# Performance work log

Hardware: AMD Instinct MI355X
Metric: run time of the kernel (lower is better)

The kernel has to match this reference:

```python
import jax, jax.numpy as jnp
import numpy as np

D = 128        # feature dim (hard-coded 128 split in source)
C = 16         # number of classes
N_S = 1600     # support set size (C * 100 shots)
Q = 32768      # number of query samples
HID = 128      # Class_Adap hidden width


def _class_centers(support_feat_inv, support_features, support_labels):
    # per-class mean of both support tensors (ComputeClassCenters)
    ones = jnp.ones((support_labels.shape[0],), support_feat_inv.dtype)
    counts = jax.ops.segment_sum(ones, support_labels, num_segments=C)
    counts = jnp.maximum(counts, 1.0)[:, None]                     # [C,1]
    mean_s = jax.ops.segment_sum(support_feat_inv, support_labels, num_segments=C) / counts   # [C,D]
    pre_s = jax.ops.segment_sum(support_features, support_labels, num_segments=C) / counts    # [C,D]
    return mean_s, pre_s


def setup_inputs() -> dict:
    key = jax.random.key(0)
    ks = jax.random.split(key, 6)
    return {
        "support_feat_inv": jax.random.normal(ks[0], (N_S, D), jnp.float32),
        "support_features": jax.random.normal(ks[1], (N_S, D), jnp.float32),
        "query_features": jax.random.normal(ks[2], (Q, D), jnp.float32),
        "W1": jax.random.normal(ks[3], (2 * D + 1, HID), jnp.float32) * 0.05,
        "b1": jnp.zeros((HID,), jnp.float32),
        "W2": jax.random.normal(ks[4], (HID, 1), jnp.float32) * 0.05,
        "b2": jnp.zeros((1,), jnp.float32),
        "support_labels": jax.random.randint(ks[5], (N_S,), 0, C),
        "query_labels": jax.random.randint(jax.random.fold_in(key, 7), (Q,), 0, C),
    }


def reference(support_feat_inv, support_features, query_features, W1, b1, W2, b2,
              support_labels, query_labels) -> jnp.ndarray:
    mean_s, pre_s = _class_centers(support_feat_inv, support_features, support_labels)
    q = query_features[:, None, :]                                  # [Q,1,D]
    gated = jax.nn.sigmoid(mean_s)[None, :, :] * q                  # [Q,C,D]
    q_full = jnp.broadcast_to(q, gated.shape)                       # [Q,C,D]
    inp = jnp.concatenate([q_full, gated], axis=-1)                 # [Q,C,2D]
    # AdaptiveAvgPool2d((None, D)) on [C,1,2D]: average adjacent pairs along last dim
    pooled = inp.reshape(Q, C, D, 2).mean(axis=-1)                  # [Q,C,D]
    # inner/outer product: sum(pre_support * query) per class
    outer = jnp.sum(pre_s[None, :, :] * q, axis=-1, keepdims=True)  # [Q,C,1]
    ext = jnp.concatenate([inp, outer], axis=-1)                    # [Q,C,2D+1]
    # Class_Adap tiny MLP -> per-class scalar weight
    h = jax.nn.relu(jnp.einsum('qce,eh->qch', ext, W1) + b1)        # [Q,C,HID]
    w = jax.nn.sigmoid(jnp.einsum('qch,ho->qco', h, W2) + b2)       # [Q,C,1]
    agg = jnp.sum(pooled * w, axis=1)                               # [Q,D]
    return agg + query_features                                     # residual (query_feature[0])
```

## Files before the change

kernel.cpp:

```cpp
#include <hip/hip_runtime.h>
#include <hip/hip_bf16.h>
#include <stdint.h>

#define DD 128
#define CC 16
#define NS 1600
#define QQ 32768
#define NBLK 64
#define PLW 65

typedef __attribute__((ext_vector_type(8))) short short8;
typedef __attribute__((ext_vector_type(4))) short short4v;
typedef __attribute__((ext_vector_type(4))) float f32x4;

__device__ inline short f2bf(float x) {
  union { float f; uint32_t u; } v; v.f = x;
  uint32_t r = (v.u + 0x7FFFu + ((v.u >> 16) & 1u)) >> 16;
  return (short)r;
}

__device__ inline uint32_t pk2bf(float lo, float hi) {
  __hip_bfloat162 h = __float22bfloat162_rn(make_float2(lo, hi));
  union { __hip_bfloat162 h2; uint32_t u; } v; v.h2 = h;
  return v.u;
}

__device__ inline float bfbits2f(uint32_t hi16bits) {
  union { uint32_t u; float f; } v; v.u = hi16bits;
  return v.f;
}

__global__ __launch_bounds__(256) void prep_kernel(
    const float* __restrict__ sfi, const float* __restrict__ sf,
    const int* __restrict__ labels, const float* __restrict__ qf,
    float* __restrict__ partA, float* __restrict__ partB,
    float* __restrict__ pcnt, short* __restrict__ qbf) {
  const int t = threadIdx.x;

  if (blockIdx.x >= NBLK) {
    const size_t cb = (size_t)(blockIdx.x - NBLK) * (128 * DD);
#pragma unroll
    for (int i = 0; i < 16; ++i) {
      const size_t off = cb + ((size_t)i * 256 + t) * 4;
      f32x4 f = *(const f32x4*)(qf + off);
      union { short4v s; uint32_t u[2]; } r;
      r.u[0] = pk2bf(f[0], f[1]);
      r.u[1] = pk2bf(f[2], f[3]);
      *(short4v*)(qbf + off) = r.s;
    }
    return;
  }

  __shared__ float accA[2][CC][DD];
  __shared__ float accB[2][CC][DD];
  __shared__ float cnt[2][CC];
  const int d = t & 127, s = t >> 7;
  for (int i = t; i < 2 * CC * DD; i += 256) {
    ((float*)accA)[i] = 0.f;
    ((float*)accB)[i] = 0.f;
  }
  if (t < 2 * CC) ((float*)cnt)[t] = 0.f;
  __syncthreads();

  const int base = blockIdx.x * (NS / NBLK);
  for (int i = s; i < NS / NBLK; i += 2) {
    const int r = base + i;
    const int lbl = labels[r];
    accA[s][lbl][d] += sfi[(size_t)r * DD + d];
    accB[s][lbl][d] += sf[(size_t)r * DD + d];
    if (d == 0) cnt[s][lbl] += 1.f;
  }
  __syncthreads();

  float* pa = partA + (size_t)blockIdx.x * (CC * DD);
  float* pb = partB + (size_t)blockIdx.x * (CC * DD);
  for (int i = t; i < CC * DD; i += 256) {
    pa[i] = ((float*)accA)[i] + ((float*)accA)[CC * DD + i];
    pb[i] = ((float*)accB)[i] + ((float*)accB)[CC * DD + i];
  }
  if (t < CC) pcnt[blockIdx.x * CC + t] = cnt[0][t] + cnt[1][t];
}

__global__ __launch_bounds__(256) void build_wt_kernel(
    const float* __restrict__ W1, const float* __restrict__ partA,
    const float* __restrict__ partB, const float* __restrict__ pcnt,
    float* __restrict__ sg_out, short* __restrict__ WtTg) {
  __shared__ float sgc[DD], prc[DD];
  const int c = blockIdx.x, t = threadIdx.x;

  float cnt = 0.f;
  for (int b = 0; b < NBLK; ++b) cnt += pcnt[b * CC + c];
  cnt = fmaxf(cnt, 1.f);
  if (t < 128) {
    float a = 0.f;
    for (int b = 0; b < NBLK; ++b) a += partA[(size_t)b * (CC * DD) + c * DD + t];
    const float m = a / cnt;
    const float s = 1.f / (1.f + expf(-m));
    sgc[t] = s;
    sg_out[c * DD + t] = s;
  } else {
    const int d = t - 128;
    float a = 0.f;
    for (int b = 0; b < NBLK; ++b) a += partB[(size_t)b * (CC * DD) + c * DD + d];
    prc[d] = a / cnt;
  }
  __syncthreads();

  for (int it = 0; it < 8; ++it) {
    const int u = it * 256 + t;
    const int w_ = u >> 8;
    const int kb = (u >> 6) & 3;
    const int lane = u & 63;
    const int j = w_ * 16 + (lane & 15);
    const int e0 = kb * 32 + (lane >> 4) * 8;
    short8 r;
#pragma unroll
    for (int rr = 0; rr < 8; ++rr) {
      const int e = e0 + rr;
      float v = W1[e * DD + j] + sgc[e] * W1[(DD + e) * DD + j] +
                prc[e] * W1[2 * DD * DD + j];
      r[rr] = f2bf(v);
    }
    *(short8*)(WtTg + ((size_t)c * 2048 + u) * 8) = r;
  }
}

__global__ __launch_bounds__(512, 4) void main_kernel(
    const short* __restrict__ qbf, const short* __restrict__ WtTg,
    const float* __restrict__ b1, const float* __restrict__ W2,
    const float* __restrict__ b2, const float* __restrict__ sg,
    float* __restrict__ out) {
  __shared__ float p_pln[4 * 64 * PLW];
  __shared__ float w_lds[64][17];

  const int tid = threadIdx.x;
  const int lane = tid & 63;
  const int w = tid >> 6;
  const int l15 = lane & 15, l4 = lane >> 4;
  const int qbase = blockIdx.x * 64;

  short8 bq[4][4];
#pragma unroll
  for (int qn = 0; qn < 4; ++qn) {
    const short* qrow = qbf + (size_t)(qbase + qn * 16 + l15) * DD;
#pragma unroll
    for (int kb = 0; kb < 4; ++kb)
      bq[qn][kb] = *(const short8*)(qrow + kb * 32 + l4 * 8);
  }

  const f32x4 b1v = *(const f32x4*)(b1 + w * 16 + l4 * 4);
  const f32x4 w2v = *(const f32x4*)(W2 + w * 16 + l4 * 4);
  const float b2s = b2[0];

  const char* wbase = (const char*)WtTg + w * 4096 + lane * 16;

#define LOADW(dst, cls)                                                     \
  {                                                                         \
    _Pragma("unroll") for (int kb = 0; kb < 4; ++kb) dst[kb] =              \
        *(const short8*)(wbase + (size_t)(cls)*32768 + kb * 1024);          \
  }

#define COMPUTE(wf, cls)                                                    \
  {                                                                         \
    const int slot = (((cls)&7) * 8 + w) * PLW + lane;                      \
    _Pragma("unroll") for (int qp = 0; qp < 2; ++qp) {                      \
      f32x4 a0 = b1v, a1 = b1v;                                             \
      _Pragma("unroll") for (int kb = 0; kb < 4; ++kb) {                    \
        a0 = __builtin_amdgcn_mfma_f32_16x16x32_bf16(wf[kb],                \
                                                     bq[2 * qp][kb], a0,    \
                                                     0, 0, 0);              \
        a1 = __builtin_amdgcn_mfma_f32_16x16x32_bf16(wf[kb],                \
                                                     bq[2 * qp + 1][kb],    \
                                                     a1, 0, 0, 0);          \
      }                                                                     \
      float p0 = 0.f, p1 = 0.f;                                             \
      _Pragma("unroll") for (int i = 0; i < 4; ++i) {                       \
        p0 += fmaxf(a0[i], 0.f) * w2v[i];                                   \
        p1 += fmaxf(a1[i], 0.f) * w2v[i];                                   \
      }                                                                     \
      p_pln[(2 * qp) * (64 * PLW) + slot] = p0;                             \
      p_pln[(2 * qp + 1) * (64 * PLW) + slot] = p1;                         \
    }                                                                       \
  }

#define REDUCE(hf)                                                          \
  {                                                                         \
    __syncthreads();                                                        \
    if (tid < 256) {                                                        \
      const int qp = tid >> 7, c7 = (tid >> 4) & 7, lr = tid & 15;          \
      _Pragma("unroll") for (int qq = 0; qq < 2; ++qq) {                    \
        const int qn = qp * 2 + qq;                                         \
        const float* pb = p_pln + qn * (64 * PLW) + c7 * (8 * PLW) + lr;    \
        float sacc = 0.f;                                                   \
        _Pragma("unroll") for (int wv = 0; wv < 8; ++wv)                    \
            _Pragma("unroll") for (int g = 0; g < 4; ++g) sacc +=           \
            pb[wv * PLW + g * 16];                                          \
        w_lds[qn * 16 + lr][(hf)*8 + c7] =                                  \
            1.f / (1.f + __expf(-(sacc + b2s)));                            \
      }                                                                     \
    }                                                                       \
    __syncthreads();                                                        \
  }

  short8 wfA[4], wfB[4];
  LOADW(wfA, 0);
  for (int cp = 0; cp < CC; cp += 2) {
    LOADW(wfB, cp + 1);
    COMPUTE(wfA, cp);
    if (cp + 2 < CC) LOADW(wfA, cp + 2);
    COMPUTE(wfB, cp + 1);
    if (cp == 6) REDUCE(0);
    if (cp == 14) REDUCE(1);
  }
#undef LOADW
#undef COMPUTE
#undef REDUCE

  {
    float2 sgv[16];
#pragma unroll
    for (int c = 0; c < 16; ++c)
      sgv[c] = *(const float2*)(sg + c * DD + 2 * lane);

#pragma unroll
    for (int qi = 0; qi < 8; ++qi) {
      const int ql = qi * 8 + w;
      const int q = qbase + ql;
      float Sv = 0.f, swx = 0.f, swy = 0.f;
#pragma unroll
      for (int c = 0; c < 16; ++c) {
        const float wc = w_lds[ql][c];
        Sv += wc;
        swx += wc * sgv[c].x;
        swy += wc * sgv[c].y;
      }
      const uint16_t* row = (const uint16_t*)(qbf + (size_t)q * DD);
      const uint32_t pair = *(const uint32_t*)(row + 2 * lane);
      const float q0 = bfbits2f(pair << 16);
      const float q1 = bfbits2f(pair & 0xFFFF0000u);
      const float qlo = bfbits2f((uint32_t)row[lane] << 16);
      const float qhi = bfbits2f((uint32_t)row[64 + lane] << 16);

      float* orow = out + (size_t)q * DD;
      orow[lane] = 0.5f * (q0 + q1) * Sv + qlo;
      orow[64 + lane] = 0.5f * (q0 * swx + q1 * swy) + qhi;
    }
  }
}

extern "C" void kernel_launch(void* const* d_in, const int* in_sizes, int n_in,
                              void* d_out, int out_size, void* d_ws, size_t ws_size,
                              hipStream_t stream) {
  const float* sfi = (const float*)d_in[0];
  const float* sf  = (const float*)d_in[1];
  const float* qf  = (const float*)d_in[2];
  const float* W1  = (const float*)d_in[3];
  const float* b1  = (const float*)d_in[4];
  const float* W2  = (const float*)d_in[5];
  const float* b2  = (const float*)d_in[6];
  const int* slab  = (const int*)d_in[7];
  float* out = (float*)d_out;

  float* sg    = (float*)d_ws;
  short* WtTg  = (short*)(sg + CC * DD);
  float* partA = (float*)(WtTg + CC * DD * DD);
  float* partB = partA + NBLK * CC * DD;
  float* pcnt  = partB + NBLK * CC * DD;
  short* qbf   = (short*)(pcnt + NBLK * CC);

  prep_kernel<<<NBLK + QQ / 128, 256, 0, stream>>>(sfi, sf, slab, qf, partA,
                                                   partB, pcnt, qbf);
  build_wt_kernel<<<CC, 256, 0, stream>>>(W1, partA, partB, pcnt, sg, WtTg);
  main_kernel<<<QQ / 64, 512, 0, stream>>>(qbf, WtTg, b1, W2, b2, sg, out);
}
```

Baseline: 53.91 us.

## Halve queries per block, reduce partials with shuffles, stagger class order per block

Each block now handles 32 queries instead of 64, which doubles the grid. The per-wave hidden-unit partial sums are reduced in registers with xor shuffles before they reach a much smaller LDS buffer. Each block starts its class loop at a different phase, so concurrent blocks read different weight slices, and the two mid-loop reductions are merged into one final reduction. The cost is that each block reloads the full class weights for half as many queries, which raises total weight traffic. The occupancy hint in launch_bounds is also dropped.

New measurement: 59.35 us. +10.1%, slower.

```diff
diff --git a/kernel.cpp b/kernel.cpp
--- a/kernel.cpp
+++ b/kernel.cpp
@@ -7,7 +7,6 @@
 #define NS 1600
 #define QQ 32768
 #define NBLK 64
-#define PLW 65
 
 typedef __attribute__((ext_vector_type(8))) short short8;
 typedef __attribute__((ext_vector_type(4))) short short4v;
@@ -125,23 +124,24 @@
   }
 }
 
-__global__ __launch_bounds__(512, 4) void main_kernel(
+__global__ __launch_bounds__(512) void main_kernel(
     const short* __restrict__ qbf, const short* __restrict__ WtTg,
     const float* __restrict__ b1, const float* __restrict__ W2,
     const float* __restrict__ b2, const float* __restrict__ sg,
     float* __restrict__ out) {
-  __shared__ float p_pln[4 * 64 * PLW];
-  __shared__ float w_lds[64][17];
+  __shared__ float p_pln[CC][8][32];
+  __shared__ float w_lds[32][17];
 
   const int tid = threadIdx.x;
   const int lane = tid & 63;
   const int w = tid >> 6;
   const int l15 = lane & 15, l4 = lane >> 4;
-  const int qbase = blockIdx.x * 64;
-
-  short8 bq[4][4];
-#pragma unroll
-  for (int qn = 0; qn < 4; ++qn) {
+  const int qbase = blockIdx.x * 32;
+  const int phase = blockIdx.x & 15;
+
+  short8 bq[2][4];
+#pragma unroll
+  for (int qn = 0; qn < 2; ++qn) {
     const short* qrow = qbf + (size_t)(qbase + qn * 16 + l15) * DD;
 #pragma unroll
     for (int kb = 0; kb < 4; ++kb)
@@ -154,67 +154,67 @@
 
   const char* wbase = (const char*)WtTg + w * 4096 + lane * 16;
 
-#define LOADW(dst, cls)                                                     \
+#define LOADW(dst, cc)                                                      \
   {                                                                         \
     _Pragma("unroll") for (int kb = 0; kb < 4; ++kb) dst[kb] =              \
-        *(const short8*)(wbase + (size_t)(cls)*32768 + kb * 1024);          \
-  }
-
-#define COMPUTE(wf, cls)                                                    \
+        *(const short8*)(wbase + (size_t)(cc)*32768 + kb * 1024);           \
+  }
+
+#define COMPUTE(wf, cc)                                                     \
   {                                                                         \
-    const int slot = (((cls)&7) * 8 + w) * PLW + lane;                      \
-    _Pragma("unroll") for (int qp = 0; qp < 2; ++qp) {                      \
-      f32x4 a0 = b1v, a1 = b1v;                                             \
-      _Pragma("unroll") for (int kb = 0; kb < 4; ++kb) {                    \
-        a0 = __builtin_amdgcn_mfma_f32_16x16x32_bf16(wf[kb],                \
-                                                     bq[2 * qp][kb], a0,    \
-                                                     0, 0, 0);              \
-        a1 = __builtin_amdgcn_mfma_f32_16x16x32_bf16(wf[kb],                \
-                                                     bq[2 * qp + 1][kb],    \
-                                                     a1, 0, 0, 0);          \
-      }                                                                     \
-      float p0 = 0.f, p1 = 0.f;                                             \
-      _Pragma("unroll") for (int i = 0; i < 4; ++i) {                       \
-        p0 += fmaxf(a0[i], 0.f) * w2v[i];                                   \
-        p1 += fmaxf(a1[i], 0.f) * w2v[i];                                   \
-      }                                                                     \
-      p_pln[(2 * qp) * (64 * PLW) + slot] = p0;                             \
-      p_pln[(2 * qp + 1) * (64 * PLW) + slot] = p1;                         \
+    f32x4 a0 = b1v, a1 = b1v;                                               \
+    _Pragma("unroll") for (int kb = 0; kb < 4; ++kb) {                      \
+      a0 = __builtin_amdgcn_mfma_f32_16x16x32_bf16(wf[kb], bq[0][kb], a0,   \
+                                                   0, 0, 0);                \
+      a1 = __builtin_amdgcn_mfma_f32_16x16x32_bf16(wf[kb], bq[1][kb], a1,   \
+                                                   0, 0, 0);                \
     }                                                                       \
-  }
-
-#define REDUCE(hf)                                                          \
-  {                                                                         \
-    __syncthreads();                                                        \
-    if (tid < 256) {                                                        \
-      const int qp = tid >> 7, c7 = (tid >> 4) & 7, lr = tid & 15;          \
-      _Pragma("unroll") for (int qq = 0; qq < 2; ++qq) {                    \
-        const int qn = qp * 2 + qq;                                         \
-        const float* pb = p_pln + qn * (64 * PLW) + c7 * (8 * PLW) + lr;    \
-        float sacc = 0.f;                                                   \
-        _Pragma("unroll") for (int wv = 0; wv < 8; ++wv)                    \
-            _Pragma("unroll") for (int g = 0; g < 4; ++g) sacc +=           \
-            pb[wv * PLW + g * 16];                                          \
-        w_lds[qn * 16 + lr][(hf)*8 + c7] =                                  \
-            1.f / (1.f + __expf(-(sacc + b2s)));                            \
-      }                                                                     \
+    float p0 = 0.f, p1 = 0.f;                                               \
+    _Pragma("unroll") for (int i = 0; i < 4; ++i) {                         \
+      p0 += fmaxf(a0[i], 0.f) * w2v[i];                                     \
+      p1 += fmaxf(a1[i], 0.f) * w2v[i];                                     \
     }                                                                       \
-    __syncthreads();                                                        \
+    p0 += __shfl_xor(p0, 16);                                               \
+    p0 += __shfl_xor(p0, 32);                                               \
+    p1 += __shfl_xor(p1, 16);                                               \
+    p1 += __shfl_xor(p1, 32);                                               \
+    if (l4 == 0) {                                                          \
+      p_pln[cc][w][l15] = p0;                                               \
+      p_pln[cc][w][16 + l15] = p1;                                          \
+    }                                                                       \
   }
 
   short8 wfA[4], wfB[4];
-  LOADW(wfA, 0);
-  for (int cp = 0; cp < CC; cp += 2) {
-    LOADW(wfB, cp + 1);
-    COMPUTE(wfA, cp);
-    if (cp + 2 < CC) LOADW(wfA, cp + 2);
-    COMPUTE(wfB, cp + 1);
-    if (cp == 6) REDUCE(0);
-    if (cp == 14) REDUCE(1);
-  }
+  LOADW(wfA, phase);
+  LOADW(wfB, (phase + 1) & 15);  COMPUTE(wfA, phase);
+  LOADW(wfA, (phase + 2) & 15);  COMPUTE(wfB, (phase + 1) & 15);
+  LOADW(wfB, (phase + 3) & 15);  COMPUTE(wfA, (phase + 2) & 15);
+  LOADW(wfA, (phase + 4) & 15);  COMPUTE(wfB, (phase + 3) & 15);
+  LOADW(wfB, (phase + 5) & 15);  COMPUTE(wfA, (phase + 4) & 15);
+  LOADW(wfA, (phase + 6) & 15);  COMPUTE(wfB, (phase + 5) & 15);
+  LOADW(wfB, (phase + 7) & 15);  COMPUTE(wfA, (phase + 6) & 15);
+  LOADW(wfA, (phase + 8) & 15);  COMPUTE(wfB, (phase + 7) & 15);
+  LOADW(wfB, (phase + 9) & 15);  COMPUTE(wfA, (phase + 8) & 15);
+  LOADW(wfA, (phase + 10) & 15); COMPUTE(wfB, (phase + 9) & 15);
+  LOADW(wfB, (phase + 11) & 15); COMPUTE(wfA, (phase + 10) & 15);
+  LOADW(wfA, (phase + 12) & 15); COMPUTE(wfB, (phase + 11) & 15);
+  LOADW(wfB, (phase + 13) & 15); COMPUTE(wfA, (phase + 12) & 15);
+  LOADW(wfA, (phase + 14) & 15); COMPUTE(wfB, (phase + 13) & 15);
+  LOADW(wfB, (phase + 15) & 15); COMPUTE(wfA, (phase + 14) & 15);
+  COMPUTE(wfB, (phase + 15) & 15);
 #undef LOADW
 #undef COMPUTE
-#undef REDUCE
+
+  __syncthreads();
+
+  {
+    const int cc = tid >> 5, rq = tid & 31;
+    float s = 0.f;
+#pragma unroll
+    for (int wv = 0; wv < 8; ++wv) s += p_pln[cc][wv][rq];
+    w_lds[rq][cc] = 1.f / (1.f + __expf(-(s + b2s)));
+  }
+  __syncthreads();
 
   {
     float2 sgv[16];
@@ -223,7 +223,7 @@
       sgv[c] = *(const float2*)(sg + c * DD + 2 * lane);
 
 #pragma unroll
-    for (int qi = 0; qi < 8; ++qi) {
+    for (int qi = 0; qi < 4; ++qi) {
       const int ql = qi * 8 + w;
       const int q = qbase + ql;
       float Sv = 0.f, swx = 0.f, swy = 0.f;
@@ -271,5 +271,5 @@
   prep_kernel<<<NBLK + QQ / 128, 256, 0, stream>>>(sfi, sf, slab, qf, partA,
                                                    partB, pcnt, qbf);
   build_wt_kernel<<<CC, 256, 0, stream>>>(W1, partA, partB, pcnt, sg, WtTg);
-  main_kernel<<<QQ / 64, 512, 0, stream>>>(qbf, WtTg, b1, W2, b2, sg, out);
-}
+  main_kernel<<<QQ / 32, 512, 0, stream>>>(qbf, WtTg, b1, W2, b2, sg, out);
+}
```
